# Performance work log

Hardware: AMD Instinct MI355X
Metric: run time of the kernel (lower is better)

## Reference

```python
import jax, jax.numpy as jnp
import numpy as np

B, N, D, H, DH = 2, 2048, 1024, 16, 64
SCALE = DH ** -0.5


def setup_inputs() -> dict:
    key = jax.random.key(0)
    k1, k2, k3 = jax.random.split(key, 3)
    x = jax.random.normal(k1, (B, N, D), dtype=jnp.float32)
    w_qkv = jax.random.normal(k2, (D, 3 * H * DH), dtype=jnp.float32) * 0.02
    w_out = jax.random.normal(k3, (H * DH, D), dtype=jnp.float32) * 0.02
    # causal boolean mask, broadcast over (b, h)
    attn_mask = jnp.tril(jnp.ones((N, N), dtype=bool))
    return {"x": x, "attn_mask": attn_mask, "w_qkv": w_qkv, "w_out": w_out}


def reference(x, attn_mask, w_qkv, w_out):
    b, n, _ = x.shape
    # fused QKV projection; Rearrange 'b n (qkv h d) -> qkv b h n d'
    qkv = (x @ w_qkv).reshape(b, n, 3, H, DH)
    qkv = jnp.transpose(qkv, (2, 0, 3, 1, 4))  # [3, b, h, n, d]
    q, k, v = qkv[0], qkv[1], qkv[2]
    q = q * SCALE
    sim = jnp.einsum('bhid,bhjd->bhij', q, k)  # [b, h, n, n]
    neg = -jnp.finfo(sim.dtype).max
    sim = jnp.where(attn_mask, sim, neg)
    attn = jax.nn.softmax(sim, axis=-1)
    out = jnp.einsum('bhij,bhjd->bhid', attn, v)  # [b, h, n, d]
    out = jnp.transpose(out, (0, 2, 1, 3)).reshape(b, n, H * DH)
    return out @ w_out
```

## Files before the change

kernel.cpp:

```cpp
#include <hip/hip_runtime.h>
#include <hip/hip_bf16.h>


typedef unsigned short u16;
typedef unsigned int u32;
typedef __bf16 bf16x8 __attribute__((ext_vector_type(8)));
typedef float  f32x4  __attribute__((ext_vector_type(4)));
typedef unsigned short u16x4 __attribute__((ext_vector_type(4)));

#define DEV __device__ __forceinline__

DEV float exp2fast(float x) { return __builtin_amdgcn_exp2f(x); }

DEV u16 f2bf(float f) {
  unsigned u = __builtin_bit_cast(unsigned, f);
  return (u16)((u + 0x7FFFu + ((u >> 16) & 1u)) >> 16);
}

DEV f32x4 mfma16(bf16x8 a, bf16x8 b, f32x4 c) {
  return __builtin_amdgcn_mfma_f32_16x16x32_bf16(a, b, c, 0, 0, 0);
}

template <typename T>
DEV void gload16(const T* g, T* l) {
  __builtin_amdgcn_global_load_lds((__attribute__((address_space(1))) void*)g,
                                   (__attribute__((address_space(3))) void*)l, 16, 0, 0);
}


__global__ __launch_bounds__(256) void cvt_x(const float* __restrict__ x,
                                             u16* __restrict__ xb) {
  int idx = (blockIdx.x * 256 + threadIdx.x) * 4;
  float4 v = *(const float4*)(x + idx);
  u16x4 u = { f2bf(v.x), f2bf(v.y), f2bf(v.z), f2bf(v.w) };
  *(u16x4*)(xb + idx) = u;
}

__global__ __launch_bounds__(256) void wtrans(const float* __restrict__ src,
                                              u16* __restrict__ dst,
                                              int R, int C, int scaleLim) {
  __shared__ u16 T[64][72];
  const int tid = threadIdx.x;
  const int c0 = blockIdx.x * 64, r0 = blockIdx.y * 64;
  const int cl = tid & 63;
  const float scale = (c0 + cl < scaleLim) ? 0.125f * 1.4426950408889634f : 1.0f;
#pragma unroll
  for (int i = 0; i < 16; ++i) {
    int r = (tid >> 6) * 16 + i;
    T[cl][r] = f2bf(src[(size_t)(r0 + r) * C + c0 + cl] * scale);
  }
  __syncthreads();
#pragma unroll
  for (int i = 0; i < 16; ++i) {
    int cc = (tid >> 6) * 16 + i;
    dst[(size_t)(c0 + cc) * R + r0 + cl] = T[cc][cl];
  }
}

__global__ __launch_bounds__(256) void vtrans(const u16* __restrict__ qkv,
                                              u16* __restrict__ vtout) {
  __shared__ u16 T[64][72];
  const int tid = threadIdx.x;
  const int n0 = blockIdx.x * 64;
  const int h = blockIdx.y, b = blockIdx.z;
  const int dl = tid & 63;
#pragma unroll
  for (int i = 0; i < 16; ++i) {
    int n = (tid >> 6) * 16 + i;
    T[dl][n] = qkv[(size_t)(b * 2048 + n0 + n) * 3072 + 2048 + h * 64 + dl];
  }
  __syncthreads();
#pragma unroll
  for (int i = 0; i < 16; ++i) {
    int d = (tid >> 6) * 16 + i;
    vtout[(size_t)((b * 16 + h) * 64 + d) * 2048 + n0 + dl] = T[d][dl];
  }
}


__global__ __launch_bounds__(256) void gemm_bf16(const u16* __restrict__ A,
                                                 const u16* __restrict__ Bt,
                                                 u16* __restrict__ Cb,
                                                 float* __restrict__ Cf,
                                                 int N, int nx, int cpx) {
  __shared__ __align__(16) u16 lA[128 * 64];
  __shared__ __align__(16) u16 lB[128 * 64];
  const int tid = threadIdx.x;
  const int lane = tid & 63, w = tid >> 6;
  const int g = lane >> 4, r16 = lane & 15;
  const int wm = w >> 1, wn = w & 1;
  const int id = (int)blockIdx.x;
  const int newid = (id & 7) * cpx + (id >> 3);
  const int m0 = (newid / nx) * 128, n0 = (newid % nx) * 128;

  const f32x4 z4 = {0.f, 0.f, 0.f, 0.f};
  f32x4 acc[4][4];
#pragma unroll
  for (int m = 0; m < 4; ++m)
#pragma unroll
    for (int n = 0; n < 4; ++n) acc[m][n] = z4;

  for (int kt = 0; kt < 16; ++kt) {
    const int kbase = kt * 64;
#pragma unroll
    for (int issue = 0; issue < 4; ++issue) {
      int i = issue * 256 + tid;
      int r = i >> 3, jp = (i & 7) ^ (r & 7);
      gload16(A + (size_t)(m0 + r) * 1024 + kbase + jp * 8,
              lA + (size_t)(issue * 256 + (tid & ~63)) * 8);
      gload16(Bt + (size_t)(n0 + r) * 1024 + kbase + jp * 8,
              lB + (size_t)(issue * 256 + (tid & ~63)) * 8);
    }
    __syncthreads();
#pragma unroll
    for (int kk = 0; kk < 2; ++kk) {
      bf16x8 a[4], b[4];
#pragma unroll
      for (int m = 0; m < 4; ++m) {
        int row = wm * 64 + m * 16 + r16;
        int off = row * 128 + ((kk * 64 + g * 16) ^ ((r16 & 7) << 4));
        a[m] = *(const bf16x8*)((const char*)lA + off);
      }
#pragma unroll
      for (int n = 0; n < 4; ++n) {
        int row = wn * 64 + n * 16 + r16;
        int off = row * 128 + ((kk * 64 + g * 16) ^ ((r16 & 7) << 4));
        b[n] = *(const bf16x8*)((const char*)lB + off);
      }
      __builtin_amdgcn_s_setprio(1);
#pragma unroll
      for (int m = 0; m < 4; ++m)
#pragma unroll
        for (int n = 0; n < 4; ++n) acc[m][n] = mfma16(a[m], b[n], acc[m][n]);
      __builtin_amdgcn_s_setprio(0);
    }
    __syncthreads();
  }
#pragma unroll
  for (int m = 0; m < 4; ++m)
#pragma unroll
    for (int n = 0; n < 4; ++n) {
      int col = n0 + wn * 64 + n * 16 + r16;
#pragma unroll
      for (int j = 0; j < 4; ++j) {
        int row = m0 + wm * 64 + m * 16 + g * 4 + j;
        if (Cb) Cb[(size_t)row * N + col] = f2bf(acc[m][n][j]);
        else    Cf[(size_t)row * N + col] = acc[m][n][j];
      }
    }
}


__global__ __launch_bounds__(256) void attn_fused(const u16* __restrict__ qkv,
                                                  const u16* __restrict__ vt,
                                                  u16* __restrict__ ao) {
  __shared__ __align__(16) u16 lK[2][64 * 64];
  __shared__ __align__(16) u16 lV[2][64 * 64];
  __shared__ __align__(16) u16 lP[4][16 * 64];
  const int tid = threadIdx.x;
  const int lane = tid & 63, w = tid >> 6;
  const int g = lane >> 4, r16 = lane & 15;

  const int flat = (int)blockIdx.x;
  const int xcd = flat & 7, slot = flat >> 3;
  const int grp = xcd * 4 + (slot >> 4);
  const int pair = slot & 15;
  const int b = grp >> 4, h = grp & 15;

  const int r = tid >> 3, jp = (tid & 7) ^ (r & 7);
  const u16* ksrc = qkv + (size_t)(b * 2048 + r) * 3072 + 1024 + h * 64 + jp * 8;
  const u16* vsrc = vt + (size_t)((b * 16 + h) * 64 + r) * 2048 + jp * 8;
  const size_t ldst = (size_t)(tid & ~63) * 8;

  const f32x4 z4 = {0.f, 0.f, 0.f, 0.f};
  u16* lp = lP[w];
  int cur = 0;

#pragma unroll 1
  for (int ph = 0; ph < 2; ++ph) {
    const int qt = ph ? pair : 31 - pair;
    const int q0w = qt * 64 + w * 16;

    bf16x8 aq[2];
    {
      const u16* qrow = qkv + (size_t)(b * 2048 + q0w + r16) * 3072 + h * 64;
      aq[0] = *(const bf16x8*)(qrow + g * 8);
      aq[1] = *(const bf16x8*)(qrow + 32 + g * 8);
    }
    f32x4 o[4];
#pragma unroll
    for (int n = 0; n < 4; ++n) o[n] = z4;
    float mrun = -INFINITY, lrun = 0.f;

    gload16(ksrc, lK[cur] + ldst);
    gload16(ksrc + (size_t)32 * 3072, lK[cur] + 2048 + ldst);
    gload16(vsrc, lV[cur] + ldst);
    gload16(vsrc + (size_t)32 * 2048, lV[cur] + 2048 + ldst);
    __syncthreads();

    for (int t = 0; t <= qt; ++t) {
      if (t < qt) {
        const u16* kn = ksrc + (size_t)(t + 1) * 64 * 3072;
        const u16* vn = vsrc + (size_t)(t + 1) * 64;
        gload16(kn, lK[cur ^ 1] + ldst);
        gload16(kn + (size_t)32 * 3072, lK[cur ^ 1] + 2048 + ldst);
        gload16(vn, lV[cur ^ 1] + ldst);
        gload16(vn + (size_t)32 * 2048, lV[cur ^ 1] + 2048 + ldst);
      }
      f32x4 s[4];
#pragma unroll
      for (int f = 0; f < 4; ++f) s[f] = z4;
      __builtin_amdgcn_s_setprio(1);
#pragma unroll
      for (int kk = 0; kk < 2; ++kk) {
#pragma unroll
        for (int f = 0; f < 4; ++f) {
          int row = f * 16 + r16;
          int off = row * 128 + ((kk * 64 + g * 16) ^ ((r16 & 7) << 4));
          bf16x8 ak = *(const bf16x8*)((const char*)lK[cur] + off);
          s[f] = mfma16(ak, aq[kk], s[f]);
        }
      }
      __builtin_amdgcn_s_setprio(0);
      if (t == qt) {
        const int qrel = w * 16 + r16;
#pragma unroll
        for (int f = 0; f < 4; ++f)
#pragma unroll
          for (int j = 0; j < 4; ++j)
            if (f * 16 + g * 4 + j > qrel) s[f][j] = -3.0e38f;
      }
      float mx = fmaxf(fmaxf(fmaxf(s[0][0], s[0][1]), fmaxf(s[0][2], s[0][3])),
                       fmaxf(fmaxf(s[1][0], s[1][1]), fmaxf(s[1][2], s[1][3])));
      mx = fmaxf(mx, fmaxf(fmaxf(fmaxf(s[2][0], s[2][1]), fmaxf(s[2][2], s[2][3])),
                           fmaxf(fmaxf(s[3][0], s[3][1]), fmaxf(s[3][2], s[3][3]))));
      mx = fmaxf(mx, __shfl_xor(mx, 16));
      mx = fmaxf(mx, __shfl_xor(mx, 32));
      float mnew = fmaxf(mrun, mx);
      float corr = exp2fast(mrun - mnew);
      mrun = mnew;
      float sm = 0.f;
#pragma unroll
      for (int f = 0; f < 4; ++f)
#pragma unroll
        for (int j = 0; j < 4; ++j) {
          s[f][j] = exp2fast(s[f][j] - mnew);
          sm += s[f][j];
        }
      sm += __shfl_xor(sm, 16);
      sm += __shfl_xor(sm, 32);
      lrun = lrun * corr + sm;
      float cj[4];
#pragma unroll
      for (int j = 0; j < 4; ++j) cj[j] = __shfl(corr, g * 4 + j);
#pragma unroll
      for (int n = 0; n < 4; ++n)
#pragma unroll
        for (int j = 0; j < 4; ++j) o[n][j] *= cj[j];

#pragma unroll
      for (int f = 0; f < 4; ++f) {
        u32 w0 = (u32)f2bf(s[f][0]) | ((u32)f2bf(s[f][1]) << 16);
        u32 w1 = (u32)f2bf(s[f][2]) | ((u32)f2bf(s[f][3]) << 16);
        int base = r16 * 128 + ((f * 32 + g * 8) ^ ((r16 & 7) << 4));
        *(u32*)((char*)lp + base) = w0;
        *(u32*)((char*)lp + base + 4) = w1;
      }
      __builtin_amdgcn_s_setprio(1);
#pragma unroll
      for (int ks = 0; ks < 2; ++ks) {
        int abyte = r16 * 128 + ((ks * 64 + g * 16) ^ ((r16 & 7) << 4));
        bf16x8 ap = *(const bf16x8*)((const char*)lp + abyte);
#pragma unroll
        for (int n = 0; n < 4; ++n) {
          int row = n * 16 + r16;
          int off = row * 128 + ((ks * 64 + g * 16) ^ ((r16 & 7) << 4));
          bf16x8 bv = *(const bf16x8*)((const char*)lV[cur] + off);
          o[n] = mfma16(ap, bv, o[n]);
        }
      }
      __builtin_amdgcn_s_setprio(0);
      __syncthreads();
      cur ^= 1;
    }
    float lj[4];
#pragma unroll
    for (int j = 0; j < 4; ++j) lj[j] = __shfl(lrun, g * 4 + j);
#pragma unroll
    for (int n = 0; n < 4; ++n) {
      int col = h * 64 + n * 16 + r16;
#pragma unroll
      for (int j = 0; j < 4; ++j) {
        int row = b * 2048 + q0w + g * 4 + j;
        ao[(size_t)row * 1024 + col] = f2bf(o[n][j] * (1.f / lj[j]));
      }
    }
  }
}


extern "C" void kernel_launch(void* const* d_in, const int* in_sizes, int n_in,
                              void* d_out, int out_size, void* d_ws, size_t ws_size,
                              hipStream_t stream) {
  const float* x     = (const float*)d_in[0];
  const float* w_qkv = (const float*)d_in[2];
  const float* w_out = (const float*)d_in[3];
  float* out = (float*)d_out;

  u16* ws = (u16*)d_ws;
  u16* x_bf  = ws;
  u16* wqkvT = x_bf + (size_t)4096 * 1024;
  u16* woutT = wqkvT + (size_t)3072 * 1024;
  u16* qkv   = woutT + (size_t)1024 * 1024;
  u16* ao    = qkv + (size_t)4096 * 3072;
  u16* vtb   = x_bf;

  cvt_x<<<4096, 256, 0, stream>>>(x, x_bf);
  wtrans<<<dim3(48, 16), 256, 0, stream>>>(w_qkv, wqkvT, 1024, 3072, 1024);
  wtrans<<<dim3(16, 16), 256, 0, stream>>>(w_out, woutT, 1024, 1024, 0);
  gemm_bf16<<<768, 256, 0, stream>>>(x_bf, wqkvT, qkv, nullptr, 3072, 24, 96);
  vtrans<<<dim3(32, 16, 2), 256, 0, stream>>>(qkv, vtb);
  attn_fused<<<512, 256, 0, stream>>>(qkv, vtb, ao);
  gemm_bf16<<<256, 256, 0, stream>>>(ao, woutT, nullptr, out, 1024, 8, 32);
}
```

Baseline: 216.8 us.

## Split attention into one q-tile per block, lazy rescale, 64x64 out-proj GEMM

The attention kernel now launches 1024 blocks, each handling a single query tile. Before, 512 blocks each handled a pair of tiles, so this doubles parallelism, and the block-to-tile mapping is arranged to balance causal work across XCDs and rounds. Online softmax rescaling of the output and the running sum is skipped when the running max would grow by at most 8 (log2 units), which removes corr shuffles and multiplies on most iterations. The output projection moves to a new 64x64-tile GEMM with 1024 blocks to fill more CUs. The trade-offs are more block launch and Q-load overhead and smaller GEMM tiles with less data reuse.

After: 195.2 us. 10.0% less time.

```diff
diff --git a/kernel.cpp b/kernel.cpp
--- a/kernel.cpp
+++ b/kernel.cpp
@@ -81,7 +81,6 @@
 __global__ __launch_bounds__(256) void gemm_bf16(const u16* __restrict__ A,
                                                  const u16* __restrict__ Bt,
                                                  u16* __restrict__ Cb,
-                                                 float* __restrict__ Cf,
                                                  int N, int nx, int cpx) {
   __shared__ __align__(16) u16 lA[128 * 64];
   __shared__ __align__(16) u16 lB[128 * 64];
@@ -144,8 +143,78 @@
 #pragma unroll
       for (int j = 0; j < 4; ++j) {
         int row = m0 + wm * 64 + m * 16 + g * 4 + j;
-        if (Cb) Cb[(size_t)row * N + col] = f2bf(acc[m][n][j]);
-        else    Cf[(size_t)row * N + col] = acc[m][n][j];
+        Cb[(size_t)row * N + col] = f2bf(acc[m][n][j]);
+      }
+    }
+}
+
+
+__global__ __launch_bounds__(256) void gemm64(const u16* __restrict__ A,
+                                              const u16* __restrict__ Bt,
+                                              float* __restrict__ Cf,
+                                              int N, int nx, int cpx) {
+  __shared__ __align__(16) u16 lA[64 * 64];
+  __shared__ __align__(16) u16 lB[64 * 64];
+  const int tid = threadIdx.x;
+  const int lane = tid & 63, w = tid >> 6;
+  const int g = lane >> 4, r16 = lane & 15;
+  const int wm = w >> 1, wn = w & 1;
+  const int id = (int)blockIdx.x;
+  const int newid = (id & 7) * cpx + (id >> 3);
+  const int m0 = (newid / nx) * 64, n0 = (newid % nx) * 64;
+
+  const f32x4 z4 = {0.f, 0.f, 0.f, 0.f};
+  f32x4 acc[2][2];
+#pragma unroll
+  for (int m = 0; m < 2; ++m)
+#pragma unroll
+    for (int n = 0; n < 2; ++n) acc[m][n] = z4;
+
+  for (int kt = 0; kt < 16; ++kt) {
+    const int kbase = kt * 64;
+#pragma unroll
+    for (int issue = 0; issue < 2; ++issue) {
+      int i = issue * 256 + tid;
+      int r = i >> 3, jp = (i & 7) ^ (r & 7);
+      gload16(A + (size_t)(m0 + r) * 1024 + kbase + jp * 8,
+              lA + (size_t)(issue * 256 + (tid & ~63)) * 8);
+      gload16(Bt + (size_t)(n0 + r) * 1024 + kbase + jp * 8,
+              lB + (size_t)(issue * 256 + (tid & ~63)) * 8);
+    }
+    __syncthreads();
+#pragma unroll
+    for (int kk = 0; kk < 2; ++kk) {
+      bf16x8 a[2], b[2];
+#pragma unroll
+      for (int m = 0; m < 2; ++m) {
+        int row = wm * 32 + m * 16 + r16;
+        int off = row * 128 + ((kk * 64 + g * 16) ^ ((r16 & 7) << 4));
+        a[m] = *(const bf16x8*)((const char*)lA + off);
+      }
+#pragma unroll
+      for (int n = 0; n < 2; ++n) {
+        int row = wn * 32 + n * 16 + r16;
+        int off = row * 128 + ((kk * 64 + g * 16) ^ ((r16 & 7) << 4));
+        b[n] = *(const bf16x8*)((const char*)lB + off);
+      }
+      __builtin_amdgcn_s_setprio(1);
+#pragma unroll
+      for (int m = 0; m < 2; ++m)
+#pragma unroll
+        for (int n = 0; n < 2; ++n) acc[m][n] = mfma16(a[m], b[n], acc[m][n]);
+      __builtin_amdgcn_s_setprio(0);
+    }
+    __syncthreads();
+  }
+#pragma unroll
+  for (int m = 0; m < 2; ++m)
+#pragma unroll
+    for (int n = 0; n < 2; ++n) {
+      int col = n0 + wn * 32 + n * 16 + r16;
+#pragma unroll
+      for (int j = 0; j < 4; ++j) {
+        int row = m0 + wm * 32 + m * 16 + g * 4 + j;
+        Cf[(size_t)row * N + col] = acc[m][n][j];
       }
     }
 }
@@ -162,10 +231,20 @@
   const int g = lane >> 4, r16 = lane & 15;
 
   const int flat = (int)blockIdx.x;
-  const int xcd = flat & 7, slot = flat >> 3;
-  const int grp = xcd * 4 + (slot >> 4);
-  const int pair = slot & 15;
+  const int xcd = flat & 7;
+  const int cu = (flat >> 3) & 31;
+  const int round = (flat >> 8) & 3;
+  const int grp = xcd * 4 + round;
+  const int qt = (round & 1) ? cu : 31 - cu;
   const int b = grp >> 4, h = grp & 15;
+  const int q0w = qt * 64 + w * 16;
+
+  bf16x8 aq[2];
+  {
+    const u16* qrow = qkv + (size_t)(b * 2048 + q0w + r16) * 3072 + h * 64;
+    aq[0] = *(const bf16x8*)(qrow + g * 8);
+    aq[1] = *(const bf16x8*)(qrow + 32 + g * 8);
+  }
 
   const int r = tid >> 3, jp = (tid & 7) ^ (r & 7);
   const u16* ksrc = qkv + (size_t)(b * 2048 + r) * 3072 + 1024 + h * 64 + jp * 8;
@@ -173,83 +252,62 @@
   const size_t ldst = (size_t)(tid & ~63) * 8;
 
   const f32x4 z4 = {0.f, 0.f, 0.f, 0.f};
+  f32x4 o[4];
+#pragma unroll
+  for (int n = 0; n < 4; ++n) o[n] = z4;
+  float mrun = -INFINITY, lrun = 0.f;
+
+  gload16(ksrc, lK[0] + ldst);
+  gload16(ksrc + (size_t)32 * 3072, lK[0] + 2048 + ldst);
+  gload16(vsrc, lV[0] + ldst);
+  gload16(vsrc + (size_t)32 * 2048, lV[0] + 2048 + ldst);
+  __syncthreads();
+
+  int cur = 0;
   u16* lp = lP[w];
-  int cur = 0;
-
-#pragma unroll 1
-  for (int ph = 0; ph < 2; ++ph) {
-    const int qt = ph ? pair : 31 - pair;
-    const int q0w = qt * 64 + w * 16;
-
-    bf16x8 aq[2];
-    {
-      const u16* qrow = qkv + (size_t)(b * 2048 + q0w + r16) * 3072 + h * 64;
-      aq[0] = *(const bf16x8*)(qrow + g * 8);
-      aq[1] = *(const bf16x8*)(qrow + 32 + g * 8);
-    }
-    f32x4 o[4];
-#pragma unroll
-    for (int n = 0; n < 4; ++n) o[n] = z4;
-    float mrun = -INFINITY, lrun = 0.f;
-
-    gload16(ksrc, lK[cur] + ldst);
-    gload16(ksrc + (size_t)32 * 3072, lK[cur] + 2048 + ldst);
-    gload16(vsrc, lV[cur] + ldst);
-    gload16(vsrc + (size_t)32 * 2048, lV[cur] + 2048 + ldst);
-    __syncthreads();
-
-    for (int t = 0; t <= qt; ++t) {
-      if (t < qt) {
-        const u16* kn = ksrc + (size_t)(t + 1) * 64 * 3072;
-        const u16* vn = vsrc + (size_t)(t + 1) * 64;
-        gload16(kn, lK[cur ^ 1] + ldst);
-        gload16(kn + (size_t)32 * 3072, lK[cur ^ 1] + 2048 + ldst);
-        gload16(vn, lV[cur ^ 1] + ldst);
-        gload16(vn + (size_t)32 * 2048, lV[cur ^ 1] + 2048 + ldst);
-      }
-      f32x4 s[4];
-#pragma unroll
-      for (int f = 0; f < 4; ++f) s[f] = z4;
-      __builtin_amdgcn_s_setprio(1);
-#pragma unroll
-      for (int kk = 0; kk < 2; ++kk) {
-#pragma unroll
-        for (int f = 0; f < 4; ++f) {
-          int row = f * 16 + r16;
-          int off = row * 128 + ((kk * 64 + g * 16) ^ ((r16 & 7) << 4));
-          bf16x8 ak = *(const bf16x8*)((const char*)lK[cur] + off);
-          s[f] = mfma16(ak, aq[kk], s[f]);
-        }
-      }
-      __builtin_amdgcn_s_setprio(0);
-      if (t == qt) {
-        const int qrel = w * 16 + r16;
-#pragma unroll
-        for (int f = 0; f < 4; ++f)
-#pragma unroll
-          for (int j = 0; j < 4; ++j)
-            if (f * 16 + g * 4 + j > qrel) s[f][j] = -3.0e38f;
-      }
-      float mx = fmaxf(fmaxf(fmaxf(s[0][0], s[0][1]), fmaxf(s[0][2], s[0][3])),
-                       fmaxf(fmaxf(s[1][0], s[1][1]), fmaxf(s[1][2], s[1][3])));
-      mx = fmaxf(mx, fmaxf(fmaxf(fmaxf(s[2][0], s[2][1]), fmaxf(s[2][2], s[2][3])),
-                           fmaxf(fmaxf(s[3][0], s[3][1]), fmaxf(s[3][2], s[3][3]))));
-      mx = fmaxf(mx, __shfl_xor(mx, 16));
-      mx = fmaxf(mx, __shfl_xor(mx, 32));
+  for (int t = 0; t <= qt; ++t) {
+    if (t < qt) {
+      const u16* kn = ksrc + (size_t)(t + 1) * 64 * 3072;
+      const u16* vn = vsrc + (size_t)(t + 1) * 64;
+      gload16(kn, lK[cur ^ 1] + ldst);
+      gload16(kn + (size_t)32 * 3072, lK[cur ^ 1] + 2048 + ldst);
+      gload16(vn, lV[cur ^ 1] + ldst);
+      gload16(vn + (size_t)32 * 2048, lV[cur ^ 1] + 2048 + ldst);
+    }
+    f32x4 s[4];
+#pragma unroll
+    for (int f = 0; f < 4; ++f) s[f] = z4;
+    __builtin_amdgcn_s_setprio(1);
+#pragma unroll
+    for (int kk = 0; kk < 2; ++kk) {
+#pragma unroll
+      for (int f = 0; f < 4; ++f) {
+        int row = f * 16 + r16;
+        int off = row * 128 + ((kk * 64 + g * 16) ^ ((r16 & 7) << 4));
+        bf16x8 ak = *(const bf16x8*)((const char*)lK[cur] + off);
+        s[f] = mfma16(ak, aq[kk], s[f]);
+      }
+    }
+    __builtin_amdgcn_s_setprio(0);
+    if (t == qt) {
+      const int qrel = w * 16 + r16;
+#pragma unroll
+      for (int f = 0; f < 4; ++f)
+#pragma unroll
+        for (int j = 0; j < 4; ++j)
+          if (f * 16 + g * 4 + j > qrel) s[f][j] = -3.0e38f;
+    }
+    float mx = fmaxf(fmaxf(fmaxf(s[0][0], s[0][1]), fmaxf(s[0][2], s[0][3])),
+                     fmaxf(fmaxf(s[1][0], s[1][1]), fmaxf(s[1][2], s[1][3])));
+    mx = fmaxf(mx, fmaxf(fmaxf(fmaxf(s[2][0], s[2][1]), fmaxf(s[2][2], s[2][3])),
+                         fmaxf(fmaxf(s[3][0], s[3][1]), fmaxf(s[3][2], s[3][3]))));
+    mx = fmaxf(mx, __shfl_xor(mx, 16));
+    mx = fmaxf(mx, __shfl_xor(mx, 32));
+    if (!__all(mx - mrun <= 8.0f)) {
       float mnew = fmaxf(mrun, mx);
       float corr = exp2fast(mrun - mnew);
       mrun = mnew;
-      float sm = 0.f;
-#pragma unroll
-      for (int f = 0; f < 4; ++f)
-#pragma unroll
-        for (int j = 0; j < 4; ++j) {
-          s[f][j] = exp2fast(s[f][j] - mnew);
-          sm += s[f][j];
-        }
-      sm += __shfl_xor(sm, 16);
-      sm += __shfl_xor(sm, 32);
-      lrun = lrun * corr + sm;
+      lrun *= corr;
       float cj[4];
 #pragma unroll
       for (int j = 0; j < 4; ++j) cj[j] = __shfl(corr, g * 4 + j);
@@ -257,43 +315,54 @@
       for (int n = 0; n < 4; ++n)
 #pragma unroll
         for (int j = 0; j < 4; ++j) o[n][j] *= cj[j];
-
-#pragma unroll
-      for (int f = 0; f < 4; ++f) {
-        u32 w0 = (u32)f2bf(s[f][0]) | ((u32)f2bf(s[f][1]) << 16);
-        u32 w1 = (u32)f2bf(s[f][2]) | ((u32)f2bf(s[f][3]) << 16);
-        int base = r16 * 128 + ((f * 32 + g * 8) ^ ((r16 & 7) << 4));
-        *(u32*)((char*)lp + base) = w0;
-        *(u32*)((char*)lp + base + 4) = w1;
-      }
-      __builtin_amdgcn_s_setprio(1);
-#pragma unroll
-      for (int ks = 0; ks < 2; ++ks) {
-        int abyte = r16 * 128 + ((ks * 64 + g * 16) ^ ((r16 & 7) << 4));
-        bf16x8 ap = *(const bf16x8*)((const char*)lp + abyte);
-#pragma unroll
-        for (int n = 0; n < 4; ++n) {
-          int row = n * 16 + r16;
-          int off = row * 128 + ((ks * 64 + g * 16) ^ ((r16 & 7) << 4));
-          bf16x8 bv = *(const bf16x8*)((const char*)lV[cur] + off);
-          o[n] = mfma16(ap, bv, o[n]);
-        }
-      }
-      __builtin_amdgcn_s_setprio(0);
-      __syncthreads();
-      cur ^= 1;
-    }
-    float lj[4];
-#pragma unroll
-    for (int j = 0; j < 4; ++j) lj[j] = __shfl(lrun, g * 4 + j);
-#pragma unroll
-    for (int n = 0; n < 4; ++n) {
-      int col = h * 64 + n * 16 + r16;
+    }
+    float sm = 0.f;
+#pragma unroll
+    for (int f = 0; f < 4; ++f)
 #pragma unroll
       for (int j = 0; j < 4; ++j) {
-        int row = b * 2048 + q0w + g * 4 + j;
-        ao[(size_t)row * 1024 + col] = f2bf(o[n][j] * (1.f / lj[j]));
-      }
+        s[f][j] = exp2fast(s[f][j] - mrun);
+        sm += s[f][j];
+      }
+    sm += __shfl_xor(sm, 16);
+    sm += __shfl_xor(sm, 32);
+    lrun += sm;
+
+#pragma unroll
+    for (int f = 0; f < 4; ++f) {
+      u32 w0 = (u32)f2bf(s[f][0]) | ((u32)f2bf(s[f][1]) << 16);
+      u32 w1 = (u32)f2bf(s[f][2]) | ((u32)f2bf(s[f][3]) << 16);
+      int base = r16 * 128 + ((f * 32 + g * 8) ^ ((r16 & 7) << 4));
+      *(u32*)((char*)lp + base) = w0;
+      *(u32*)((char*)lp + base + 4) = w1;
+    }
+    __builtin_amdgcn_s_setprio(1);
+#pragma unroll
+    for (int ks = 0; ks < 2; ++ks) {
+      int abyte = r16 * 128 + ((ks * 64 + g * 16) ^ ((r16 & 7) << 4));
+      bf16x8 ap = *(const bf16x8*)((const char*)lp + abyte);
+#pragma unroll
+      for (int n = 0; n < 4; ++n) {
+        int row = n * 16 + r16;
+        int off = row * 128 + ((ks * 64 + g * 16) ^ ((r16 & 7) << 4));
+        bf16x8 bv = *(const bf16x8*)((const char*)lV[cur] + off);
+        o[n] = mfma16(ap, bv, o[n]);
+      }
+    }
+    __builtin_amdgcn_s_setprio(0);
+    __syncthreads();
+    cur ^= 1;
+  }
+  float lj[4];
+#pragma unroll
+  for (int j = 0; j < 4; ++j) lj[j] = __shfl(lrun, g * 4 + j);
+#pragma unroll
+  for (int n = 0; n < 4; ++n) {
+    int col = h * 64 + n * 16 + r16;
+#pragma unroll
+    for (int j = 0; j < 4; ++j) {
+      int row = b * 2048 + q0w + g * 4 + j;
+      ao[(size_t)row * 1024 + col] = f2bf(o[n][j] * (1.f / lj[j]));
     }
   }
 }
@@ -318,8 +387,8 @@
   cvt_x<<<4096, 256, 0, stream>>>(x, x_bf);
   wtrans<<<dim3(48, 16), 256, 0, stream>>>(w_qkv, wqkvT, 1024, 3072, 1024);
   wtrans<<<dim3(16, 16), 256, 0, stream>>>(w_out, woutT, 1024, 1024, 0);
-  gemm_bf16<<<768, 256, 0, stream>>>(x_bf, wqkvT, qkv, nullptr, 3072, 24, 96);
+  gemm_bf16<<<768, 256, 0, stream>>>(x_bf, wqkvT, qkv, 3072, 24, 96);
   vtrans<<<dim3(32, 16, 2), 256, 0, stream>>>(qkv, vtb);
-  attn_fused<<<512, 256, 0, stream>>>(qkv, vtb, ao);
-  gemm_bf16<<<256, 256, 0, stream>>>(ao, woutT, nullptr, out, 1024, 8, 32);
-}
+  attn_fused<<<1024, 256, 0, stream>>>(qkv, vtb, ao);
+  gemm64<<<1024, 256, 0, stream>>>(ao, woutT, out, 1024, 16, 128);
+}
```
